# Performance work log

Hardware: AMD Instinct MI355X
Metric: run time of the kernel (lower is better)

The kernel has to match this reference:

```python
import jax, jax.numpy as jnp
import numpy as np
import math

H = 256
NH = 8
HD = H // NH
FF = 2 * H
NSESS = 8
LN_EPS = 1e-5


def _layernorm(x, g, b):
    m = jnp.mean(x, axis=-1, keepdims=True)
    v = jnp.mean((x - m) ** 2, axis=-1, keepdims=True)
    return (x - m) / jnp.sqrt(v + LN_EPS) * g + b


def setup_inputs() -> dict:
    key = jax.random.key(0)
    ks = jax.random.split(key, 32)
    B, S, N = 4, 256, 32
    inp = {
        'sequence': jax.random.normal(ks[0], (B, S, N, H), dtype=jnp.float32),
        'regime_signal': jax.random.normal(ks[1], (B, S), dtype=jnp.float32),
        'session_transition': jax.random.normal(ks[2], (B, S), dtype=jnp.float32),
    }
    w = lambda k, shape: jax.random.normal(k, shape, dtype=jnp.float32) * 0.02
    inp['q_w'] = w(ks[3], (H, H)); inp['q_b'] = jnp.zeros((H,), jnp.float32)
    inp['k_w'] = w(ks[4], (H, H)); inp['k_b'] = jnp.zeros((H,), jnp.float32)
    inp['v_w'] = w(ks[5], (H, H)); inp['v_b'] = jnp.zeros((H,), jnp.float32)
    inp['o_w'] = w(ks[6], (H, H)); inp['o_b'] = jnp.zeros((H,), jnp.float32)
    inp['sess_emb'] = w(ks[7], (NSESS, H))
    inp['reg_w'] = w(ks[8], (H,)); inp['reg_b'] = jnp.zeros((H,), jnp.float32)
    inp['tr_w'] = w(ks[9], (H,)); inp['tr_b'] = jnp.zeros((H,), jnp.float32)
    inp['tq_w'] = w(ks[10], (H, H)); inp['tq_b'] = jnp.zeros((H,), jnp.float32)
    inp['tk_w'] = w(ks[11], (H, H)); inp['tk_b'] = jnp.zeros((H,), jnp.float32)
    inp['ff_w1'] = w(ks[12], (H, FF)); inp['ff_b1'] = jnp.zeros((FF,), jnp.float32)
    inp['ff_w2'] = w(ks[13], (FF, H)); inp['ff_b2'] = jnp.zeros((H,), jnp.float32)
    inp['ln1_g'] = jnp.ones((H,), jnp.float32); inp['ln1_b'] = jnp.zeros((H,), jnp.float32)
    inp['ln2_g'] = jnp.ones((H,), jnp.float32); inp['ln2_b'] = jnp.zeros((H,), jnp.float32)
    inp['valid_mask'] = jax.random.randint(ks[14], (B, S, N), 0, 2).astype(bool)
    inp['session_codes'] = jax.random.randint(ks[15], (B, S), 0, NSESS).astype(jnp.int64)
    return inp


def _forward(sequence, regime_signal, session_transition,
             q_w, q_b, k_w, k_b, v_w, v_b, o_w, o_b,
             sess_emb, reg_w, reg_b, tr_w, tr_b,
             tq_w, tq_b, tk_w, tk_b,
             ff_w1, ff_b1, ff_w2, ff_b2,
             ln1_g, ln1_b, ln2_g, ln2_b,
             valid_mask, session_codes):
    B, S, N, Hd = sequence.shape
    BN = B * N
    # [B,S,N,H] -> [B*N, S, H]
    flat = sequence.transpose(0, 2, 1, 3).reshape(BN, S, Hd)

    # time-state: session embedding + regime/transition scalar projections
    sess = jnp.clip(session_codes, 0, NSESS - 1)
    sess_flat = jnp.broadcast_to(sess[:, None, :], (B, N, S)).reshape(BN, S)
    time_state = sess_emb[sess_flat]  # [BN, S, H]
    reg_flat = jnp.broadcast_to(regime_signal[:, None, :], (B, N, S)).reshape(BN, S)
    time_state = time_state + reg_flat[..., None] * reg_w + reg_b
    tr_flat = jnp.broadcast_to(session_transition[:, None, :], (B, N, S)).reshape(BN, S)
    time_state = time_state + tr_flat[..., None] * tr_w + tr_b

    def heads(x):  # [BN,S,H] -> [BN,NH,S,HD]
        return x.reshape(BN, S, NH, HD).transpose(0, 2, 1, 3)

    q = heads((flat + time_state) @ q_w + q_b)
    k = heads((flat + time_state) @ k_w + k_b)
    v = heads(flat @ v_w + v_b)
    tq = heads(time_state @ tq_w + tq_b)
    tk = heads(time_state @ tk_w + tk_b)

    scale = 1.0 / math.sqrt(float(HD))
    scores = jnp.einsum('bhqd,bhkd->bhqk', q, k) * scale
    scores = scores + 0.25 * jnp.einsum('bhqd,bhkd->bhqk', tq, tk) * scale

    causal = jnp.triu(jnp.ones((S, S), dtype=bool), k=1)
    scores = jnp.where(causal[None, None], -10000.0, scores)

    valid = valid_mask.transpose(0, 2, 1).reshape(BN, S)  # [BN,S]
    all_invalid = ~jnp.any(valid, axis=1)  # [BN]
    scores = jnp.where(~valid[:, None, None, :], -10000.0, scores)
    first_key = (jnp.arange(S) == 0)
    scores = jnp.where(all_invalid[:, None, None, None] & first_key, 0.0, scores)

    attn = jax.nn.softmax(scores, axis=-1)
    attn = attn * valid[:, None, None, :].astype(attn.dtype)
    attn = attn / jnp.maximum(jnp.sum(attn, axis=-1, keepdims=True), 1e-6)
    attn = jnp.where(all_invalid[:, None, None, None], 0.0, attn)

    attn_out = jnp.einsum('bhqk,bhkd->bhqd', attn, v)
    attn_out = attn_out.transpose(0, 2, 1, 3).reshape(BN, S, Hd)
    attn_out = attn_out @ o_w + o_b

    x = _layernorm(flat + attn_out, ln1_g, ln1_b)  # dropout identity (eval / p=0)
    ff = jax.nn.gelu(x @ ff_w1 + ff_b1, approximate=False) @ ff_w2 + ff_b2
    x = _layernorm(x + ff, ln2_g, ln2_b)
    x = x * valid[..., None].astype(x.dtype)
    return x.reshape(B, N, S, Hd).transpose(0, 2, 1, 3)  # [B,S,N,H]


def reference(sequence, regime_signal, session_transition,
              q_w, q_b, k_w, k_b, v_w, v_b, o_w, o_b,
              sess_emb, reg_w, reg_b, tr_w, tr_b,
              tq_w, tq_b, tk_w, tk_b,
              ff_w1, ff_b1, ff_w2, ff_b2,
              ln1_g, ln1_b, ln2_g, ln2_b,
              valid_mask, session_codes):
    return _forward(sequence, regime_signal, session_transition,
                    q_w, q_b, k_w, k_b, v_w, v_b, o_w, o_b,
                    sess_emb, reg_w, reg_b, tr_w, tr_b,
                    tq_w, tq_b, tk_w, tk_b,
                    ff_w1, ff_b1, ff_w2, ff_b2,
                    ln1_g, ln1_b, ln2_g, ln2_b,
                    valid_mask, session_codes)
```

## Files before the change

### kernel.cpp

```cpp
#include <hip/hip_runtime.h>
#include <math.h>

#define B_ 4
#define S_ 256
#define N_ 32
#define H_ 256
#define NH_ 8
#define HD_ 32
#define FF_ 512
#define BN_ 128
#define M_ 32768
#define BS_ 1024

typedef __attribute__((ext_vector_type(8))) short short8;
typedef __attribute__((ext_vector_type(4))) short short4v;
typedef __attribute__((ext_vector_type(4))) float f32x4;
typedef __attribute__((ext_vector_type(16))) float f32x16;
typedef __attribute__((ext_vector_type(4))) int i32x4;

__device__ __forceinline__ unsigned short f2bf(float f) {
  unsigned u = __builtin_bit_cast(unsigned, f);
  u = (u + 0x7FFFu + ((u >> 16) & 1u)) >> 16;
  return (unsigned short)u;
}
__device__ __forceinline__ float bf2f(unsigned short h) {
  unsigned u = ((unsigned)h) << 16;
  return __builtin_bit_cast(float, u);
}

__device__ __forceinline__ void gload16(const void* g, void* l) {
  __builtin_amdgcn_global_load_lds(
      (const __attribute__((address_space(1))) unsigned*)g,
      (__attribute__((address_space(3))) unsigned*)l, 16, 0, 0);
}

__global__ __launch_bounds__(256)
void ts_kernel(const float* __restrict__ reg, const float* __restrict__ tr,
               const int* __restrict__ codes,
               const float* __restrict__ sess_emb,
               const float* __restrict__ reg_w, const float* __restrict__ reg_b,
               const float* __restrict__ tr_w, const float* __restrict__ tr_b,
               float* __restrict__ ts) {
  const int bs = blockIdx.x;
  const int h = threadIdx.x;
  int c = codes[bs];
  c = c < 0 ? 0 : (c > 7 ? 7 : c);
  const float r = reg[bs], t = tr[bs];
  ts[bs * H_ + h] = sess_emb[c * H_ + h] + r * reg_w[h] + reg_b[h]
                    + t * tr_w[h] + tr_b[h];
}

__global__ __launch_bounds__(256)
void cvtall_kernel(const float* __restrict__ q_w, const float* __restrict__ k_w,
                   const float* __restrict__ v_w, const float* __restrict__ o_w,
                   const float* __restrict__ tq_w, const float* __restrict__ tk_w,
                   const float* __restrict__ ff1_w, const float* __restrict__ ff2_w,
                   unsigned short* __restrict__ wqk, unsigned short* __restrict__ wv,
                   unsigned short* __restrict__ wo, unsigned short* __restrict__ wtqtk,
                   unsigned short* __restrict__ wff1, unsigned short* __restrict__ wff2) {
  const int bid = blockIdx.x, tid = threadIdx.x;
  const float* src; unsigned short* dst; int ns, K, base;
  if (bid < 256)       { src = q_w;   dst = wqk;           ns = 8; K = 256; base = 0; }
  else if (bid < 512)  { src = k_w;   dst = wqk + 65536;   ns = 8; K = 256; base = 256; }
  else if (bid < 768)  { src = v_w;   dst = wv;            ns = 8; K = 256; base = 512; }
  else if (bid < 1024) { src = o_w;   dst = wo;            ns = 8; K = 256; base = 768; }
  else if (bid < 1280) { src = tq_w;  dst = wtqtk;         ns = 8; K = 256; base = 1024; }
  else if (bid < 1536) { src = tk_w;  dst = wtqtk + 65536; ns = 8; K = 256; base = 1280; }
  else if (bid < 2048) { src = ff1_w; dst = wff1;          ns = 9; K = 256; base = 1536; }
  else                 { src = ff2_w; dst = wff2;          ns = 8; K = 512; base = 2048; }
  const int idx = (bid - base) * 256 + tid;
  const int k = idx >> ns, n = idx & ((1 << ns) - 1);
  dst[n * K + k] = f2bf(src[idx]);
}

__global__ __launch_bounds__(256)
void prep_kernel(const float* __restrict__ seq, const float* __restrict__ ts,
                 unsigned short* __restrict__ flatb, unsigned short* __restrict__ fpb) {
  const int row = blockIdx.x * 8 + (threadIdx.x >> 5);
  const int c0 = (threadIdx.x & 31) * 8;
  const int bn = row >> 8, s = row & 255;
  const int b = bn >> 5, n = bn & 31;
  const float* sp = &seq[((((b << 8) + s) << 5) + n) * 256 + c0];
  const float* tp = &ts[(((b << 8) + s) << 8) + c0];
  const float4 a0 = *(const float4*)sp, a1 = *(const float4*)(sp + 4);
  const float4 t0 = *(const float4*)tp, t1 = *(const float4*)(tp + 4);
  short8 fv, gv;
  fv[0] = (short)f2bf(a0.x); fv[1] = (short)f2bf(a0.y);
  fv[2] = (short)f2bf(a0.z); fv[3] = (short)f2bf(a0.w);
  fv[4] = (short)f2bf(a1.x); fv[5] = (short)f2bf(a1.y);
  fv[6] = (short)f2bf(a1.z); fv[7] = (short)f2bf(a1.w);
  gv[0] = (short)f2bf(a0.x + t0.x); gv[1] = (short)f2bf(a0.y + t0.y);
  gv[2] = (short)f2bf(a0.z + t0.z); gv[3] = (short)f2bf(a0.w + t0.w);
  gv[4] = (short)f2bf(a1.x + t1.x); gv[5] = (short)f2bf(a1.y + t1.y);
  gv[6] = (short)f2bf(a1.z + t1.z); gv[7] = (short)f2bf(a1.w + t1.w);
  *(short8*)&flatb[row * 256 + c0] = fv;
  *(short8*)&fpb[row * 256 + c0] = gv;
}

template<int AMODE, int RESMODE, bool GELU_, int K, int NOUT, bool OUTBF,
         bool DUALB, bool SCALEH>
__global__ __launch_bounds__(256)
void mmb_kernel(const void* __restrict__ Av, const unsigned short* __restrict__ Wt,
                const float* __restrict__ bias, const float* __restrict__ bias2,
                const unsigned short* __restrict__ resb,
                void* __restrict__ Cv, float post_scale) {
  constexpr int LDA = (AMODE == 3) ? 64 : 72;
  constexpr int LDB = (AMODE == 3) ? 64 : 72;
  __shared__ unsigned short As[128 * 72];
  __shared__ unsigned short Bs[128 * 72];
  const int tid = threadIdx.x;
  const int m0 = blockIdx.x * 128, n0 = blockIdx.y * 128;
  const int l = tid & 63, w = tid >> 6;
  const int wr = w >> 1, wc = w & 1;
  const int lr = l & 15, lg = l >> 4;
  f32x4 acc[4][4] = {};

  const unsigned short* ga = nullptr;
  const unsigned short* gb = nullptr;
  if (AMODE == 3) {
    ga = (const unsigned short*)Av + (m0 + w * 32 + (l >> 3)) * K + (l & 7) * 8;
    gb = Wt + (n0 + w * 32 + (l >> 3)) * K + (l & 7) * 8;
  }

  for (int k0 = 0; k0 < K; k0 += 64) {
    if (AMODE == 3) {
#pragma unroll
      for (int i = 0; i < 4; ++i) {
        gload16(ga + k0 + i * 8 * K, &As[(w * 32 + i * 8) * 64]);
        gload16(gb + k0 + i * 8 * K, &Bs[(w * 32 + i * 8) * 64]);
      }
    } else {
#pragma unroll
      for (int i = 0; i < 8; ++i) {
        const int seg = i * 256 + tid;
        const int r = seg >> 4, c4 = (seg & 15) * 4;
        const float4 a4 = *(const float4*)&((const float*)Av)[(m0 + r) * K + k0 + c4];
        short4v sv;
        sv[0] = (short)f2bf(a4.x); sv[1] = (short)f2bf(a4.y);
        sv[2] = (short)f2bf(a4.z); sv[3] = (short)f2bf(a4.w);
        *(short4v*)&As[r * LDA + c4] = sv;
      }
#pragma unroll
      for (int i = 0; i < 4; ++i) {
        const int seg = i * 256 + tid;
        const int n = seg >> 3, c8 = (seg & 7) * 8;
        const short8 v = *(const short8*)&Wt[(n0 + n) * K + k0 + c8];
        *(short8*)&Bs[n * LDB + c8] = v;
      }
    }
    __syncthreads();
#pragma unroll
    for (int ks = 0; ks < 2; ++ks) {
      short8 af[4], bfr[4];
#pragma unroll
      for (int qt = 0; qt < 4; ++qt)
        af[qt] = *(const short8*)&As[(wr * 64 + qt * 16 + lr) * LDA + ks * 32 + lg * 8];
#pragma unroll
      for (int nt = 0; nt < 4; ++nt)
        bfr[nt] = *(const short8*)&Bs[(wc * 64 + nt * 16 + lr) * LDB + ks * 32 + lg * 8];
#pragma unroll
      for (int qt = 0; qt < 4; ++qt)
#pragma unroll
        for (int nt = 0; nt < 4; ++nt)
          acc[qt][nt] = __builtin_amdgcn_mfma_f32_16x16x32_bf16(
              af[qt], bfr[nt], acc[qt][nt], 0, 0, 0);
    }
    __syncthreads();
  }

#pragma unroll
  for (int qt = 0; qt < 4; ++qt) {
#pragma unroll
    for (int nt = 0; nt < 4; ++nt) {
      const int col = n0 + wc * 64 + nt * 16 + lr;
      const float bsv = DUALB ? (col < 256 ? bias[col] : bias2[col - 256])
                              : bias[col];
      const float sc = SCALEH ? (col < 256 ? post_scale : 1.0f) : post_scale;
#pragma unroll
      for (int i = 0; i < 4; ++i) {
        const int row = m0 + wr * 64 + qt * 16 + (lg << 2) + i;
        float v = (acc[qt][nt][i] + bsv) * sc;
        if (RESMODE == 2) v += bf2f(resb[row * NOUT + col]);
        if (GELU_) v = 0.5f * v * (1.0f + erff(v * 0.70710678118654752f));
        if (OUTBF) ((unsigned short*)Cv)[row * NOUT + col] = f2bf(v);
        else       ((float*)Cv)[row * NOUT + col] = v;
      }
    }
  }
}

__global__ __launch_bounds__(512, 4)
void attn4_kernel(const unsigned short* __restrict__ qkb,
                  const unsigned short* __restrict__ vb,
                  const unsigned short* __restrict__ tqtkb,
                  const int* __restrict__ valid,
                  unsigned short* __restrict__ ao) {
  __shared__ __align__(16) char KsB[256 * 128];
  __shared__ __align__(16) char VsB[32 * 512];

  const int bn = blockIdx.x & 127;
  const int h = blockIdx.x >> 7;
  const int b = bn >> 5, n = bn & 31;
  const int tid = threadIdx.x, l = tid & 63, w = tid >> 6;
  const int lq = l & 31, hi = l >> 5;
  const int qa = w * 32 + lq;

  const unsigned long long bm0 = __ballot(valid[((b << 8) + 0   + l) * 32 + n] != 0);
  const unsigned long long bm1 = __ballot(valid[((b << 8) + 64  + l) * 32 + n] != 0);
  const unsigned long long bm2 = __ballot(valid[((b << 8) + 128 + l) * 32 + n] != 0);
  const unsigned long long bm3 = __ballot(valid[((b << 8) + 192 + l) * 32 + n] != 0);

  short8 qf[4];
  {
    const unsigned short* qp = &qkb[((bn << 8) + qa) * 512 + (h << 5)];
    const unsigned short* tp = &tqtkb[((b << 8) + qa) * 512 + (h << 5)];
    qf[0] = *(const short8*)&qp[hi * 8];
    qf[1] = *(const short8*)&qp[16 + hi * 8];
    qf[2] = *(const short8*)&tp[hi * 8];
    qf[3] = *(const short8*)&tp[16 + hi * 8];
  }

#pragma unroll
  for (int i = 0; i < 4; ++i) {
    const int e = i * 512 + tid;
    const int key = e >> 3, c = e & 7;
    const unsigned short* src = (c < 4)
        ? &qkb[((bn << 8) + key) * 512 + 256 + (h << 5) + c * 8]
        : &tqtkb[((b << 8) + key) * 512 + 256 + (h << 5) + (c - 4) * 8];
    *(short8*)(KsB + key * 128 + ((c * 16) ^ ((key & 7) << 4))) = *(const short8*)src;
  }
#pragma unroll
  for (int i = 0; i < 2; ++i) {
    const int e = i * 512 + tid;
    const int key = e >> 2, c = e & 3;
    const short8 v = *(const short8*)&vb[((bn << 8) + key) * 256 + (h << 5) + c * 8];
#pragma unroll
    for (int j = 0; j < 8; ++j) {
      const int dv = c * 8 + j;
      *(unsigned short*)(VsB + dv * 512 + ((key * 2) ^ ((dv & 7) << 4))) =
          (unsigned short)v[j];
    }
  }
  __syncthreads();

  f32x16 oacc = {};
  float lrun = 0.0f;

  for (int g = 0; g <= w; ++g) {
    const int kbase = g << 5;
    f32x16 s = {};
#pragma unroll
    for (int df = 0; df < 4; ++df) {
      const int key = kbase + lq;
      const short8 akf = *(const short8*)(
          KsB + key * 128 + ((df * 32 + hi * 16) ^ ((key & 7) << 4)));
      s = __builtin_amdgcn_mfma_f32_32x32x16_bf16(akf, qf[df], s, 0, 0, 0);
    }
    const unsigned long long bmc = (kbase < 64) ? bm0 : (kbase < 128) ? bm1
                                 : (kbase < 192) ? bm2 : bm3;
    const unsigned wnd = (kbase & 32) ? (unsigned)(bmc >> 32) : (unsigned)bmc;
    float p[16];
#pragma unroll
    for (int r = 0; r < 16; ++r) {
      const int crow = (r & 3) + 8 * (r >> 2) + 4 * hi;
      const int key = kbase + crow;
      const bool ok = (key <= qa) && (((wnd >> crow) & 1u) != 0u);
      p[r] = ok ? __builtin_amdgcn_exp2f(s[r]) : 0.0f;
    }
    float rs = ((p[0] + p[1]) + (p[2] + p[3])) + ((p[4] + p[5]) + (p[6] + p[7]))
             + ((p[8] + p[9]) + (p[10] + p[11])) + ((p[12] + p[13]) + (p[14] + p[15]));
    rs += __shfl_xor(rs, 32);
    lrun += rs;
    unsigned wds[8];
#pragma unroll
    for (int i2 = 0; i2 < 8; ++i2)
      wds[i2] = (unsigned)f2bf(p[2 * i2]) | ((unsigned)f2bf(p[2 * i2 + 1]) << 16);
    unsigned xw[8];
#pragma unroll
    for (int i2 = 0; i2 < 8; ++i2)
      xw[i2] = (unsigned)__shfl_xor((int)wds[i2], 32);
    i32x4 f0, f1;
    f0[0] = (int)(hi ? xw[2] : wds[0]);
    f0[1] = (int)(hi ? xw[3] : wds[1]);
    f0[2] = (int)(hi ? wds[2] : xw[0]);
    f0[3] = (int)(hi ? wds[3] : xw[1]);
    f1[0] = (int)(hi ? xw[6] : wds[4]);
    f1[1] = (int)(hi ? xw[7] : wds[5]);
    f1[2] = (int)(hi ? wds[6] : xw[4]);
    f1[3] = (int)(hi ? wds[7] : xw[5]);
    const short8 pf0 = __builtin_bit_cast(short8, f0);
    const short8 pf1 = __builtin_bit_cast(short8, f1);
    {
      const short8 avf = *(const short8*)(
          VsB + lq * 512 + (((kbase + hi * 8) * 2) ^ ((lq & 7) << 4)));
      oacc = __builtin_amdgcn_mfma_f32_32x32x16_bf16(avf, pf0, oacc, 0, 0, 0);
    }
    {
      const short8 avf = *(const short8*)(
          VsB + lq * 512 + (((kbase + 16 + hi * 8) * 2) ^ ((lq & 7) << 4)));
      oacc = __builtin_amdgcn_mfma_f32_32x32x16_bf16(avf, pf1, oacc, 0, 0, 0);
    }
  }


  const float inv = 1.0f / fmaxf(lrun, 1e-6f);
  const int row = (bn << 8) + qa;
#pragma unroll
  for (int g2 = 0; g2 < 4; ++g2) {
    const unsigned long long h0 = f2bf(oacc[4 * g2 + 0] * inv);
    const unsigned long long h1 = f2bf(oacc[4 * g2 + 1] * inv);
    const unsigned long long h2 = f2bf(oacc[4 * g2 + 2] * inv);
    const unsigned long long h3 = f2bf(oacc[4 * g2 + 3] * inv);
    const unsigned long long pkt = h0 | (h1 << 16) | (h2 << 32) | (h3 << 48);
    *(unsigned long long*)&ao[row * 256 + (h << 5) + 8 * g2 + 4 * hi] = pkt;
  }
}

__global__ __launch_bounds__(256)
void ln1_kernel(const float* __restrict__ X, const float* __restrict__ g,
                const float* __restrict__ bb, unsigned short* __restrict__ out) {
  const int row = blockIdx.x * 4 + (threadIdx.x >> 6);
  const int lane = threadIdx.x & 63;
  const float4 x = *(const float4*)&X[row * 256 + lane * 4];
  float s1 = x.x + x.y + x.z + x.w;
#pragma unroll
  for (int off = 1; off < 64; off <<= 1) s1 += __shfl_xor(s1, off);
  const float mean = s1 * (1.0f / 256.0f);
  const float dx = x.x - mean, dy = x.y - mean, dz = x.z - mean, dw = x.w - mean;
  float s2 = dx * dx + dy * dy + dz * dz + dw * dw;
#pragma unroll
  for (int off = 1; off < 64; off <<= 1) s2 += __shfl_xor(s2, off);
  const float rstd = rsqrtf(s2 * (1.0f / 256.0f) + 1e-5f);
  const int c0 = lane * 4;
  short4v y;
  y[0] = (short)f2bf(dx * rstd * g[c0] + bb[c0]);
  y[1] = (short)f2bf(dy * rstd * g[c0 + 1] + bb[c0 + 1]);
  y[2] = (short)f2bf(dz * rstd * g[c0 + 2] + bb[c0 + 2]);
  y[3] = (short)f2bf(dw * rstd * g[c0 + 3] + bb[c0 + 3]);
  *(short4v*)&out[row * 256 + c0] = y;
}

__global__ __launch_bounds__(256)
void ln2_kernel(const float* __restrict__ X, const float* __restrict__ g,
                const float* __restrict__ bb, float* __restrict__ out,
                const int* __restrict__ valid) {
  const int row = blockIdx.x * 4 + (threadIdx.x >> 6);
  const int lane = threadIdx.x & 63;
  const float4 x = *(const float4*)&X[row * 256 + lane * 4];
  float s1 = x.x + x.y + x.z + x.w;
#pragma unroll
  for (int off = 1; off < 64; off <<= 1) s1 += __shfl_xor(s1, off);
  const float mean = s1 * (1.0f / 256.0f);
  const float dx = x.x - mean, dy = x.y - mean, dz = x.z - mean, dw = x.w - mean;
  float s2 = dx * dx + dy * dy + dz * dz + dw * dw;
#pragma unroll
  for (int off = 1; off < 64; off <<= 1) s2 += __shfl_xor(s2, off);
  const float rstd = rsqrtf(s2 * (1.0f / 256.0f) + 1e-5f);
  const int c0 = lane * 4;
  const int bn = row >> 8, s = row & 255;
  const int b = bn >> 5, n = bn & 31;
  const float vmv = (valid[((b << 8) + s) * 32 + n] != 0) ? 1.0f : 0.0f;
  float4 y;
  y.x = (dx * rstd * g[c0] + bb[c0]) * vmv;
  y.y = (dy * rstd * g[c0 + 1] + bb[c0 + 1]) * vmv;
  y.z = (dz * rstd * g[c0 + 2] + bb[c0 + 2]) * vmv;
  y.w = (dw * rstd * g[c0 + 3] + bb[c0 + 3]) * vmv;
  *(float4*)&out[(((((b << 8) + s) << 5) + n) << 8) + c0] = y;
}

extern "C" void kernel_launch(void* const* d_in, const int* in_sizes, int n_in,
                              void* d_out, int out_size, void* d_ws, size_t ws_size,
                              hipStream_t stream) {
  const float* seq    = (const float*)d_in[0];
  const float* regs   = (const float*)d_in[1];
  const float* trs    = (const float*)d_in[2];
  const float* q_w    = (const float*)d_in[3];
  const float* q_b    = (const float*)d_in[4];
  const float* k_w    = (const float*)d_in[5];
  const float* k_b    = (const float*)d_in[6];
  const float* v_w    = (const float*)d_in[7];
  const float* v_b    = (const float*)d_in[8];
  const float* o_w    = (const float*)d_in[9];
  const float* o_b    = (const float*)d_in[10];
  const float* semb   = (const float*)d_in[11];
  const float* reg_w  = (const float*)d_in[12];
  const float* reg_b  = (const float*)d_in[13];
  const float* tr_w   = (const float*)d_in[14];
  const float* tr_b   = (const float*)d_in[15];
  const float* tq_w   = (const float*)d_in[16];
  const float* tq_b   = (const float*)d_in[17];
  const float* tk_w   = (const float*)d_in[18];
  const float* tk_b   = (const float*)d_in[19];
  const float* ff_w1  = (const float*)d_in[20];
  const float* ff_b1  = (const float*)d_in[21];
  const float* ff_w2  = (const float*)d_in[22];
  const float* ff_b2  = (const float*)d_in[23];
  const float* ln1_g  = (const float*)d_in[24];
  const float* ln1_b  = (const float*)d_in[25];
  const float* ln2_g  = (const float*)d_in[26];
  const float* ln2_b  = (const float*)d_in[27];
  const int*   valid  = (const int*)d_in[28];
  const int*   codes  = (const int*)d_in[29];

  float* f32ws = (float*)d_ws;
  float* ts    = f32ws;
  float* x1pre = f32ws + 262144;
  unsigned short* bws = (unsigned short*)(f32ws + 262144 + 8388608);
  unsigned short* flatb = bws;
  unsigned short* fpb   = bws + 8388608;
  unsigned short* qkb   = bws + 16777216;
  unsigned short* vb    = bws + 33554432;
  unsigned short* tqtkb = bws + 41943040;
  unsigned short* wqk   = bws + 42467328;
  unsigned short* wv    = bws + 42598400;
  unsigned short* wo    = bws + 42663936;
  unsigned short* wtqtk = bws + 42729472;
  unsigned short* wff1  = bws + 42860544;
  unsigned short* wff2  = bws + 42991616;
  unsigned short* ao  = fpb;
  unsigned short* x1b = flatb;
  unsigned short* h1  = qkb;
  float* x2 = x1pre;
  float* outp = (float*)d_out;

  const float c2 = 0.25505402f;

  ts_kernel<<<BS_, 256, 0, stream>>>(regs, trs, codes, semb, reg_w, reg_b,
                                     tr_w, tr_b, ts);
  cvtall_kernel<<<2560, 256, 0, stream>>>(q_w, k_w, v_w, o_w, tq_w, tk_w,
                                          ff_w1, ff_w2, wqk, wv, wo, wtqtk,
                                          wff1, wff2);
  prep_kernel<<<M_ / 8, 256, 0, stream>>>(seq, ts, flatb, fpb);
  mmb_kernel<0, 0, false, 256, 512, true, true, true>
      <<<dim3(8, 4), 256, 0, stream>>>(ts, wtqtk, tq_b, tk_b, nullptr,
                                       tqtkb, 0.25f * c2);
  mmb_kernel<3, 0, false, 256, 512, true, true, true>
      <<<dim3(256, 4), 256, 0, stream>>>(fpb, wqk, q_b, k_b, nullptr,
                                         qkb, c2);
  mmb_kernel<3, 0, false, 256, 256, true, false, false>
      <<<dim3(256, 2), 256, 0, stream>>>(flatb, wv, v_b, nullptr, nullptr,
                                         vb, 1.0f);
  attn4_kernel<<<BN_ * NH_, 512, 0, stream>>>(qkb, vb, tqtkb, valid, ao);
  mmb_kernel<3, 2, false, 256, 256, false, false, false>
      <<<dim3(256, 2), 256, 0, stream>>>(ao, wo, o_b, nullptr, flatb,
                                         x1pre, 1.0f);
  ln1_kernel<<<M_ / 4, 256, 0, stream>>>(x1pre, ln1_g, ln1_b, x1b);
  mmb_kernel<3, 0, true, 256, 512, true, false, false>
      <<<dim3(256, 4), 256, 0, stream>>>(x1b, wff1, ff_b1, nullptr, nullptr,
                                         h1, 1.0f);
  mmb_kernel<3, 2, false, 512, 256, false, false, false>
      <<<dim3(256, 2), 256, 0, stream>>>(h1, wff2, ff_b2, nullptr, x1b,
                                         x2, 1.0f);
  ln2_kernel<<<M_ / 4, 256, 0, stream>>>(x2, ln2_g, ln2_b, outp, valid);
}
```

Baseline: 190.5 us.

## Fuse output and FFN2 GEMMs with residual add and LayerNorm

Adds a gemmln kernel that computes a 64-row by 256-column GEMM tile, adds bias and the bf16 residual, and does the LayerNorm reduction in-block through warp shuffles plus a small shared-memory cross-wave sum. It replaces the out-projection GEMM plus ln1 and the FFN2 GEMM plus ln2 (with valid masking and output transpose). This removes the fp32 intermediate write and re-read and two kernel launches. In exchange the GEMM is a simpler single-buffered tile with unswizzled LDS and scalar epilogue stores, and variance is computed as E[x^2]-mean^2.

```diff
diff --git a/kernel.cpp b/kernel.cpp
--- a/kernel.cpp
+++ b/kernel.cpp
@@ -189,6 +189,112 @@
   }
 }
 
+template<int K, bool FINAL>
+__global__ __launch_bounds__(256, 2)
+void gemmln_kernel(const unsigned short* __restrict__ Ab,
+                   const unsigned short* __restrict__ Wt,
+                   const float* __restrict__ bias,
+                   const unsigned short* __restrict__ resb,
+                   const float* __restrict__ g, const float* __restrict__ bb,
+                   const int* __restrict__ valid,
+                   void* __restrict__ out) {
+  __shared__ unsigned short As[64 * 64];
+  __shared__ unsigned short Bs[256 * 64];
+  __shared__ float Red[4][64][2];
+  const int tid = threadIdx.x;
+  const int m0 = blockIdx.x * 64;
+  const int l = tid & 63, w = tid >> 6;
+  const int lr = l & 15, lg = l >> 4;
+  f32x4 acc[4][4] = {};
+
+  const unsigned short* ga = Ab + (m0 + w * 16 + (l >> 3)) * K + (l & 7) * 8;
+  const unsigned short* gb = Wt + (w * 64 + (l >> 3)) * K + (l & 7) * 8;
+
+  for (int k0 = 0; k0 < K; k0 += 64) {
+#pragma unroll
+    for (int i = 0; i < 2; ++i)
+      gload16(ga + k0 + i * 8 * K, &As[(w * 16 + i * 8) * 64]);
+#pragma unroll
+    for (int i = 0; i < 8; ++i)
+      gload16(gb + k0 + i * 8 * K, &Bs[(w * 64 + i * 8) * 64]);
+    __syncthreads();
+#pragma unroll
+    for (int ks = 0; ks < 2; ++ks) {
+      short8 af[4], bfr[4];
+#pragma unroll
+      for (int qt = 0; qt < 4; ++qt)
+        af[qt] = *(const short8*)&As[(qt * 16 + lr) * 64 + ks * 32 + lg * 8];
+#pragma unroll
+      for (int nt = 0; nt < 4; ++nt)
+        bfr[nt] = *(const short8*)&Bs[(w * 64 + nt * 16 + lr) * 64 + ks * 32 + lg * 8];
+#pragma unroll
+      for (int qt = 0; qt < 4; ++qt)
+#pragma unroll
+        for (int nt = 0; nt < 4; ++nt)
+          acc[qt][nt] = __builtin_amdgcn_mfma_f32_16x16x32_bf16(
+              af[qt], bfr[nt], acc[qt][nt], 0, 0, 0);
+    }
+    __syncthreads();
+  }
+
+#pragma unroll
+  for (int qt = 0; qt < 4; ++qt) {
+#pragma unroll
+    for (int i = 0; i < 4; ++i) {
+      const int rl = qt * 16 + (lg << 2) + i;
+      const int row = m0 + rl;
+      float s1 = 0.0f, s2 = 0.0f;
+#pragma unroll
+      for (int nt = 0; nt < 4; ++nt) {
+        const int col = w * 64 + nt * 16 + lr;
+        float v = acc[qt][nt][i] + bias[col] + bf2f(resb[row * 256 + col]);
+        acc[qt][nt][i] = v;
+        s1 += v; s2 += v * v;
+      }
+      s1 += __shfl_xor(s1, 1); s2 += __shfl_xor(s2, 1);
+      s1 += __shfl_xor(s1, 2); s2 += __shfl_xor(s2, 2);
+      s1 += __shfl_xor(s1, 4); s2 += __shfl_xor(s2, 4);
+      s1 += __shfl_xor(s1, 8); s2 += __shfl_xor(s2, 8);
+      if (lr == 0) { Red[w][rl][0] = s1; Red[w][rl][1] = s2; }
+    }
+  }
+  __syncthreads();
+
+#pragma unroll
+  for (int qt = 0; qt < 4; ++qt) {
+#pragma unroll
+    for (int i = 0; i < 4; ++i) {
+      const int rl = qt * 16 + (lg << 2) + i;
+      const int row = m0 + rl;
+      const float s1 = (Red[0][rl][0] + Red[1][rl][0])
+                     + (Red[2][rl][0] + Red[3][rl][0]);
+      const float s2 = (Red[0][rl][1] + Red[1][rl][1])
+                     + (Red[2][rl][1] + Red[3][rl][1]);
+      const float mean = s1 * (1.0f / 256.0f);
+      const float var = s2 * (1.0f / 256.0f) - mean * mean;
+      const float rstd = rsqrtf(var + 1e-5f);
+      if (FINAL) {
+        const int bn = row >> 8, s = row & 255;
+        const int b = bn >> 5, n = bn & 31;
+        const float vm = (valid[((b << 8) + s) * 32 + n] != 0) ? 1.0f : 0.0f;
+        float* op = (float*)out + ((((b << 8) + s) << 5) + n) * 256;
+#pragma unroll
+        for (int nt = 0; nt < 4; ++nt) {
+          const int col = w * 64 + nt * 16 + lr;
+          op[col] = ((acc[qt][nt][i] - mean) * rstd * g[col] + bb[col]) * vm;
+        }
+      } else {
+        unsigned short* op = (unsigned short*)out + row * 256;
+#pragma unroll
+        for (int nt = 0; nt < 4; ++nt) {
+          const int col = w * 64 + nt * 16 + lr;
+          op[col] = f2bf((acc[qt][nt][i] - mean) * rstd * g[col] + bb[col]);
+        }
+      }
+    }
+  }
+}
+
 __global__ __launch_bounds__(512, 4)
 void attn4_kernel(const unsigned short* __restrict__ qkb,
                   const unsigned short* __restrict__ vb,
@@ -302,7 +408,6 @@
     }
   }
 
-
   const float inv = 1.0f / fmaxf(lrun, 1e-6f);
   const int row = (bn << 8) + qa;
 #pragma unroll
@@ -314,58 +419,6 @@
     const unsigned long long pkt = h0 | (h1 << 16) | (h2 << 32) | (h3 << 48);
     *(unsigned long long*)&ao[row * 256 + (h << 5) + 8 * g2 + 4 * hi] = pkt;
   }
-}
-
-__global__ __launch_bounds__(256)
-void ln1_kernel(const float* __restrict__ X, const float* __restrict__ g,
-                const float* __restrict__ bb, unsigned short* __restrict__ out) {
-  const int row = blockIdx.x * 4 + (threadIdx.x >> 6);
-  const int lane = threadIdx.x & 63;
-  const float4 x = *(const float4*)&X[row * 256 + lane * 4];
-  float s1 = x.x + x.y + x.z + x.w;
-#pragma unroll
-  for (int off = 1; off < 64; off <<= 1) s1 += __shfl_xor(s1, off);
-  const float mean = s1 * (1.0f / 256.0f);
-  const float dx = x.x - mean, dy = x.y - mean, dz = x.z - mean, dw = x.w - mean;
-  float s2 = dx * dx + dy * dy + dz * dz + dw * dw;
-#pragma unroll
-  for (int off = 1; off < 64; off <<= 1) s2 += __shfl_xor(s2, off);
-  const float rstd = rsqrtf(s2 * (1.0f / 256.0f) + 1e-5f);
-  const int c0 = lane * 4;
-  short4v y;
-  y[0] = (short)f2bf(dx * rstd * g[c0] + bb[c0]);
-  y[1] = (short)f2bf(dy * rstd * g[c0 + 1] + bb[c0 + 1]);
-  y[2] = (short)f2bf(dz * rstd * g[c0 + 2] + bb[c0 + 2]);
-  y[3] = (short)f2bf(dw * rstd * g[c0 + 3] + bb[c0 + 3]);
-  *(short4v*)&out[row * 256 + c0] = y;
-}
-
-__global__ __launch_bounds__(256)
-void ln2_kernel(const float* __restrict__ X, const float* __restrict__ g,
-                const float* __restrict__ bb, float* __restrict__ out,
-                const int* __restrict__ valid) {
-  const int row = blockIdx.x * 4 + (threadIdx.x >> 6);
-  const int lane = threadIdx.x & 63;
-  const float4 x = *(const float4*)&X[row * 256 + lane * 4];
-  float s1 = x.x + x.y + x.z + x.w;
-#pragma unroll
-  for (int off = 1; off < 64; off <<= 1) s1 += __shfl_xor(s1, off);
-  const float mean = s1 * (1.0f / 256.0f);
-  const float dx = x.x - mean, dy = x.y - mean, dz = x.z - mean, dw = x.w - mean;
-  float s2 = dx * dx + dy * dy + dz * dz + dw * dw;
-#pragma unroll
-  for (int off = 1; off < 64; off <<= 1) s2 += __shfl_xor(s2, off);
-  const float rstd = rsqrtf(s2 * (1.0f / 256.0f) + 1e-5f);
-  const int c0 = lane * 4;
-  const int bn = row >> 8, s = row & 255;
-  const int b = bn >> 5, n = bn & 31;
-  const float vmv = (valid[((b << 8) + s) * 32 + n] != 0) ? 1.0f : 0.0f;
-  float4 y;
-  y.x = (dx * rstd * g[c0] + bb[c0]) * vmv;
-  y.y = (dy * rstd * g[c0 + 1] + bb[c0 + 1]) * vmv;
-  y.z = (dz * rstd * g[c0 + 2] + bb[c0 + 2]) * vmv;
-  y.w = (dw * rstd * g[c0 + 3] + bb[c0 + 3]) * vmv;
-  *(float4*)&out[(((((b << 8) + s) << 5) + n) << 8) + c0] = y;
 }
 
 extern "C" void kernel_launch(void* const* d_in, const int* in_sizes, int n_in,
@@ -404,7 +457,6 @@
 
   float* f32ws = (float*)d_ws;
   float* ts    = f32ws;
-  float* x1pre = f32ws + 262144;
   unsigned short* bws = (unsigned short*)(f32ws + 262144 + 8388608);
   unsigned short* flatb = bws;
   unsigned short* fpb   = bws + 8388608;
@@ -420,7 +472,6 @@
   unsigned short* ao  = fpb;
   unsigned short* x1b = flatb;
   unsigned short* h1  = qkb;
-  float* x2 = x1pre;
   float* outp = (float*)d_out;
 
   const float c2 = 0.25505402f;
@@ -441,15 +492,11 @@
       <<<dim3(256, 2), 256, 0, stream>>>(flatb, wv, v_b, nullptr, nullptr,
                                          vb, 1.0f);
   attn4_kernel<<<BN_ * NH_, 512, 0, stream>>>(qkb, vb, tqtkb, valid, ao);
-  mmb_kernel<3, 2, false, 256, 256, false, false, false>
-      <<<dim3(256, 2), 256, 0, stream>>>(ao, wo, o_b, nullptr, flatb,
-                                         x1pre, 1.0f);
-  ln1_kernel<<<M_ / 4, 256, 0, stream>>>(x1pre, ln1_g, ln1_b, x1b);
+  gemmln_kernel<256, false><<<M_ / 64, 256, 0, stream>>>(
+      ao, wo, o_b, flatb, ln1_g, ln1_b, nullptr, x1b);
   mmb_kernel<3, 0, true, 256, 512, true, false, false>
       <<<dim3(256, 4), 256, 0, stream>>>(x1b, wff1, ff_b1, nullptr, nullptr,
                                          h1, 1.0f);
-  mmb_kernel<3, 2, false, 512, 256, false, false, false>
-      <<<dim3(256, 2), 256, 0, stream>>>(h1, wff2, ff_b2, nullptr, x1b,
-                                         x2, 1.0f);
-  ln2_kernel<<<M_ / 4, 256, 0, stream>>>(x2, ln2_g, ln2_b, outp, valid);
-}
+  gemmln_kernel<512, true><<<M_ / 64, 256, 0, stream>>>(
+      h1, wff2, ff_b2, x1b, ln2_g, ln2_b, valid, outp);
+}
```

Result: faster. 172.5 us (-9.5%).
